# Optimization experiments

Hardware: AMD Instinct MI355X
Metric: run time of the kernel (lower is better)

## Reference

```python
import jax, jax.numpy as jnp
import numpy as np

D = 1024
H = 16
HD = D // H
E = 64
K = 2


def setup_inputs() -> dict:
    key = jax.random.key(0)
    ks = jax.random.split(key, 10)
    s = 0.02
    return {
        "x": jax.random.normal(ks[0], (8, 2048, D), dtype=jnp.float32),
        "expert_embeddings": jax.random.normal(ks[1], (E, D), dtype=jnp.float32),
        "in_proj_w": jax.random.normal(ks[2], (3 * D, D), dtype=jnp.float32) * s,
        "in_proj_b": jax.random.normal(ks[3], (3 * D,), dtype=jnp.float32) * s,
        "out_proj_w": jax.random.normal(ks[4], (D, D), dtype=jnp.float32) * s,
        "out_proj_b": jax.random.normal(ks[5], (D,), dtype=jnp.float32) * s,
        "gate_w1": jax.random.normal(ks[6], (4 * E, D), dtype=jnp.float32) * s,
        "gate_b1": jax.random.normal(ks[7], (4 * E,), dtype=jnp.float32) * s,
        "gate_w2": jax.random.normal(ks[8], (E, 4 * E), dtype=jnp.float32) * s,
        "gate_b2": jax.random.normal(ks[9], (E,), dtype=jnp.float32) * s,
    }


def reference(x, expert_embeddings, in_proj_w, in_proj_b, out_proj_w, out_proj_b,
              gate_w1, gate_b1, gate_w2, gate_b2):
    B, S, _ = x.shape
    wq, wk, wv = jnp.split(in_proj_w, 3, axis=0)   # each (D, D)
    bq, bk, bv = jnp.split(in_proj_b, 3, axis=0)
    # cross-attention: queries from x, keys/values from expert embeddings (shared across batch)
    q = (x @ wq.T + bq).reshape(B, S, H, HD)                      # (B,S,H,hd)
    k = (expert_embeddings @ wk.T + bk).reshape(E, H, HD)         # (E,H,hd)
    v = (expert_embeddings @ wv.T + bv).reshape(E, H, HD)
    scores = jnp.einsum('bshd,ehd->bhse', q, k) / jnp.sqrt(jnp.float32(HD))
    attn = jax.nn.softmax(scores, axis=-1)                        # (B,H,S,E)
    o = jnp.einsum('bhse,ehd->bshd', attn, v).reshape(B, S, D)
    attn_out = o @ out_proj_w.T + out_proj_b                      # (B,S,D)
    # gate MLP (exact GELU like torch default)
    h = jax.nn.gelu(attn_out @ gate_w1.T + gate_b1, approximate=False)
    gate_logits = h @ gate_w2.T + gate_b2                         # (B,S,E)
    probs = jax.nn.softmax(gate_logits, axis=-1)
    vals, idx = jax.lax.top_k(probs, K)                           # (B,S,K)
    weights = vals / (jnp.sum(vals, axis=-1, keepdims=True) + 1e-8)
    return idx, weights
```

## Files before the change

### kernel.cpp

```cpp
#include <hip/hip_runtime.h>
#include <math.h>


typedef _Float16 h8 __attribute__((ext_vector_type(8)));
typedef _Float16 h4 __attribute__((ext_vector_type(4)));
typedef float f4 __attribute__((ext_vector_type(4)));

__device__ __forceinline__ float gelu_exact(float x) {
    return 0.5f * x * (1.0f + erff(x * 0.70710678118654752f));
}

__global__ __launch_bounds__(256) void split2_kernel(
    const float* __restrict__ src, _Float16* __restrict__ dst, long total, int colsh) {
    long i = ((long)blockIdx.x * 256 + threadIdx.x) * 4;
    if (i >= total) return;
    f4 v = *(const f4*)(src + i);
    long row = i >> colsh; int col = (int)(i & ((1 << colsh) - 1));
    _Float16* d0 = dst + (row << (colsh + 1)) + col;
    h4 lo, hi;
    #pragma unroll
    for (int j = 0; j < 4; j++) {
        _Float16 a = (_Float16)v[j];
        lo[j] = a;
        hi[j] = (_Float16)((v[j] - (float)a) * 4096.0f);
    }
    *(h4*)d0 = lo;
    *(h4*)(d0 + (1 << colsh)) = hi;
}

__global__ __launch_bounds__(256) void kv_kernel(
    const float* __restrict__ w, const float* __restrict__ b,
    const float* __restrict__ ee, float* __restrict__ kbuf, float* __restrict__ vtbuf) {
    __shared__ float As[32][68];
    __shared__ float Bs[32][68];
    int tid = threadIdx.x;
    int r0 = blockIdx.x * 64;
    int tx = tid & 15, ty = tid >> 4;
    float acc[4][4] = {};
    const float* wbase = w + (size_t)(1024 + r0) * 1024;
    for (int k0 = 0; k0 < 1024; k0 += 32) {
        #pragma unroll
        for (int i = 0; i < 2; i++) {
            int f = tid + i * 256;
            int row = f >> 3, c4 = f & 7;
            float4 v = *(const float4*)(wbase + (size_t)row * 1024 + k0 + c4 * 4);
            As[c4*4+0][row] = v.x; As[c4*4+1][row] = v.y;
            As[c4*4+2][row] = v.z; As[c4*4+3][row] = v.w;
            float4 u = *(const float4*)(ee + (size_t)row * 1024 + k0 + c4 * 4);
            Bs[c4*4+0][row] = u.x; Bs[c4*4+1][row] = u.y;
            Bs[c4*4+2][row] = u.z; Bs[c4*4+3][row] = u.w;
        }
        __syncthreads();
        #pragma unroll
        for (int kk = 0; kk < 32; kk++) {
            float a[4], bb[4];
            *(float4*)&a[0]  = *(const float4*)&As[kk][ty * 4];
            *(float4*)&bb[0] = *(const float4*)&Bs[kk][tx * 4];
            #pragma unroll
            for (int i = 0; i < 4; i++)
                #pragma unroll
                for (int j = 0; j < 4; j++)
                    acc[i][j] = fmaf(a[i], bb[j], acc[i][j]);
        }
        __syncthreads();
    }
    #pragma unroll
    for (int i = 0; i < 4; i++) {
        int row = r0 + ty * 4 + i;
        float bias = b[1024 + row];
        int j = row & 1023;
        int h = j >> 6, hd = j & 63;
        #pragma unroll
        for (int jj = 0; jj < 4; jj++) {
            int e = tx * 4 + jj;
            float val = acc[i][jj] + bias;
            if (row < 1024) kbuf[h * 4096 + e * 64 + hd] = val;
            else            vtbuf[h * 4096 + hd * 64 + e] = val;
        }
    }
}

template<int GELU, int OSPLIT, int AF32>
__global__ __launch_bounds__(256, 2) void hgemm_kernel(
    const void* __restrict__ Av, const _Float16* __restrict__ B,
    const float* __restrict__ bias, void* __restrict__ Cv, int ldc, int nhalf) {
    __shared__ __align__(16) _Float16 As[128 * 32];
    __shared__ __align__(16) _Float16 Ah[128 * 32];
    __shared__ __align__(16) _Float16 Bl[128 * 32];
    __shared__ __align__(16) _Float16 Bh[128 * 32];
    int tid = threadIdx.x;

    int gx = gridDim.x;
    int nwg = gx * gridDim.y;
    int lid = blockIdx.y * gx + blockIdx.x;
    int L = (lid & 7) * (nwg >> 3) + (lid >> 3);
    int m0 = (L / gx) * 128, n0 = (L % gx) * 128;

    int w = tid >> 6, l = tid & 63;
    int wm = w & 1, wn = w >> 1;
    int lr = l & 15, lk = l >> 4;

    f4 acc1[4][4], acc2[4][4];
    #pragma unroll
    for (int i = 0; i < 4; i++)
        #pragma unroll
        for (int j = 0; j < 4; j++) {
            acc1[i][j] = (f4){0.f, 0.f, 0.f, 0.f};
            acc2[i][j] = (f4){0.f, 0.f, 0.f, 0.f};
        }

    int r0 = tid >> 2, c0 = tid & 3;
    int s0 = r0 * 32 + c0 * 8, s1 = s0 + 64 * 32;
    int rb = tid >> 3, c4 = tid & 7;

    const _Float16* Ab = (const _Float16*)Av + (size_t)m0 * 2048;
    const float*    Af = (const float*)Av + (size_t)m0 * 1024;
    const _Float16* Bb = B + (size_t)n0 * 2048;

    float4 xa[4];
    uint4 ua0, ua1, uh0, uh1, ub0, ub1, uc0, uc1;
    if (AF32) {
        #pragma unroll
        for (int f = 0; f < 4; f++)
            xa[f] = *(const float4*)(Af + (size_t)(rb + f * 32) * 1024 + c4 * 4);
    } else {
        ua0 = *(const uint4*)(Ab + (size_t)r0 * 2048 + c0 * 8);
        ua1 = *(const uint4*)(Ab + (size_t)(r0 + 64) * 2048 + c0 * 8);
        uh0 = *(const uint4*)(Ab + (size_t)r0 * 2048 + 1024 + c0 * 8);
        uh1 = *(const uint4*)(Ab + (size_t)(r0 + 64) * 2048 + 1024 + c0 * 8);
    }
    ub0 = *(const uint4*)(Bb + (size_t)r0 * 2048 + c0 * 8);
    ub1 = *(const uint4*)(Bb + (size_t)(r0 + 64) * 2048 + c0 * 8);
    uc0 = *(const uint4*)(Bb + (size_t)r0 * 2048 + 1024 + c0 * 8);
    uc1 = *(const uint4*)(Bb + (size_t)(r0 + 64) * 2048 + 1024 + c0 * 8);

    for (int kt = 0; kt < 32; kt++) {
        __syncthreads();
        if (AF32) {
            #pragma unroll
            for (int f = 0; f < 4; f++) {
                h4 lo, hi;
                #pragma unroll
                for (int j = 0; j < 4; j++) {
                    float v = ((const float*)&xa[f])[j];
                    _Float16 a = (_Float16)v;
                    lo[j] = a;
                    hi[j] = (_Float16)((v - (float)a) * 4096.0f);
                }
                *(h4*)(As + (rb + f * 32) * 32 + c4 * 4) = lo;
                *(h4*)(Ah + (rb + f * 32) * 32 + c4 * 4) = hi;
            }
        } else {
            *(uint4*)(As + s0) = ua0; *(uint4*)(As + s1) = ua1;
            *(uint4*)(Ah + s0) = uh0; *(uint4*)(Ah + s1) = uh1;
        }
        *(uint4*)(Bl + s0) = ub0; *(uint4*)(Bl + s1) = ub1;
        *(uint4*)(Bh + s0) = uc0; *(uint4*)(Bh + s1) = uc1;
        __syncthreads();
        if (kt < 31) {
            int ka = (kt + 1) * 32;
            if (AF32) {
                #pragma unroll
                for (int f = 0; f < 4; f++)
                    xa[f] = *(const float4*)(Af + (size_t)(rb + f * 32) * 1024 + ka + c4 * 4);
            } else {
                ua0 = *(const uint4*)(Ab + (size_t)r0 * 2048 + ka + c0 * 8);
                ua1 = *(const uint4*)(Ab + (size_t)(r0 + 64) * 2048 + ka + c0 * 8);
                uh0 = *(const uint4*)(Ab + (size_t)r0 * 2048 + 1024 + ka + c0 * 8);
                uh1 = *(const uint4*)(Ab + (size_t)(r0 + 64) * 2048 + 1024 + ka + c0 * 8);
            }
            ub0 = *(const uint4*)(Bb + (size_t)r0 * 2048 + ka + c0 * 8);
            ub1 = *(const uint4*)(Bb + (size_t)(r0 + 64) * 2048 + ka + c0 * 8);
            uc0 = *(const uint4*)(Bb + (size_t)r0 * 2048 + 1024 + ka + c0 * 8);
            uc1 = *(const uint4*)(Bb + (size_t)(r0 + 64) * 2048 + 1024 + ka + c0 * 8);
        }
        h8 a1f[4], blf[4], bhf[4];
        #pragma unroll
        for (int mi = 0; mi < 4; mi++)
            a1f[mi] = *(const h8*)(As + (wm * 64 + mi * 16 + lr) * 32 + lk * 8);
        #pragma unroll
        for (int ni = 0; ni < 4; ni++) {
            blf[ni] = *(const h8*)(Bl + (wn * 64 + ni * 16 + lr) * 32 + lk * 8);
            bhf[ni] = *(const h8*)(Bh + (wn * 64 + ni * 16 + lr) * 32 + lk * 8);
        }
        #pragma unroll
        for (int mi = 0; mi < 4; mi++)
            #pragma unroll
            for (int ni = 0; ni < 4; ni++) {
                acc1[mi][ni] = __builtin_amdgcn_mfma_f32_16x16x32_f16(a1f[mi], blf[ni], acc1[mi][ni], 0, 0, 0);
                acc2[mi][ni] = __builtin_amdgcn_mfma_f32_16x16x32_f16(a1f[mi], bhf[ni], acc2[mi][ni], 0, 0, 0);
            }
        h8 a2f[4];
        #pragma unroll
        for (int mi = 0; mi < 4; mi++)
            a2f[mi] = *(const h8*)(Ah + (wm * 64 + mi * 16 + lr) * 32 + lk * 8);
        #pragma unroll
        for (int mi = 0; mi < 4; mi++)
            #pragma unroll
            for (int ni = 0; ni < 4; ni++)
                acc2[mi][ni] = __builtin_amdgcn_mfma_f32_16x16x32_f16(a2f[mi], blf[ni], acc2[mi][ni], 0, 0, 0);
    }

    #pragma unroll
    for (int mi = 0; mi < 4; mi++)
        #pragma unroll
        for (int ni = 0; ni < 4; ni++) {
            int n = n0 + wn * 64 + ni * 16 + lr;
            float bn = bias[n];
            #pragma unroll
            for (int j = 0; j < 4; j++) {
                int m = m0 + wm * 64 + mi * 16 + lk * 4 + j;
                float val = acc1[mi][ni][j] + acc2[mi][ni][j] * (1.0f / 4096.0f) + bn;
                if (GELU) val = gelu_exact(val);
                if (OSPLIT) {
                    _Float16* Ch = (_Float16*)Cv;
                    _Float16 lo = (_Float16)val;
                    Ch[(size_t)m * ldc + n] = lo;
                    Ch[(size_t)m * ldc + nhalf + n] = (_Float16)((val - (float)lo) * 4096.0f);
                } else {
                    ((float*)Cv)[(size_t)m * ldc + n] = val;
                }
            }
        }
}

__global__ __launch_bounds__(256) void attn2_kernel(
    const float* __restrict__ kbuf, const float* __restrict__ vtbuf,
    const float* __restrict__ q, _Float16* __restrict__ os) {
    __shared__ __align__(16) float qs[4][64][68];
    __shared__ __align__(16) float ps[4][2][64];
    int tid = threadIdx.x;
    int w = tid >> 6, l = tid & 63;
    int wid = blockIdx.x * 4 + w;
    int b = wid >> 9, h = (wid >> 5) & 15, t0 = (wid & 31) * 64;

    f4 kr[16], vt[16];
    const f4* kp = (const f4*)(kbuf + h * 4096 + l * 64);
    const f4* vp = (const f4*)(vtbuf + h * 4096 + l * 64);
    #pragma unroll
    for (int i = 0; i < 16; i++) { kr[i] = kp[i]; vt[i] = vp[i]; }

    const float* qbase = q + ((size_t)(b * 2048 + t0)) * 1024 + h * 64;
    #pragma unroll
    for (int it = 0; it < 16; it++) {
        int f = it * 64 + l;
        int r = f >> 4, c = f & 15;
        f4 v = *(const f4*)(qbase + (size_t)r * 1024 + c * 4);
        *(f4*)&qs[w][r][c * 4] = v;
    }

    for (int t = 0; t < 64; t++) {
        float s = 0.f;
        #pragma unroll
        for (int i = 0; i < 16; i++) {
            f4 qv = *(const f4*)&qs[w][t][i * 4];
            s = fmaf(qv[0], kr[i][0], s);
            s = fmaf(qv[1], kr[i][1], s);
            s = fmaf(qv[2], kr[i][2], s);
            s = fmaf(qv[3], kr[i][3], s);
        }
        s *= 0.125f;
        float ex = __expf(s);
        float sum = ex;
        #pragma unroll
        for (int off = 32; off; off >>= 1) sum += __shfl_xor(sum, off, 64);
        float p = ex / sum;
        ps[w][t & 1][l] = p;
        float o = 0.f;
        #pragma unroll
        for (int i = 0; i < 16; i++) {
            f4 pv = *(const f4*)&ps[w][t & 1][i * 4];
            o = fmaf(pv[0], vt[i][0], o);
            o = fmaf(pv[1], vt[i][1], o);
            o = fmaf(pv[2], vt[i][2], o);
            o = fmaf(pv[3], vt[i][3], o);
        }
        _Float16 o1 = (_Float16)o;
        _Float16 o2 = (_Float16)((o - (float)o1) * 4096.0f);
        size_t tok = (size_t)(b * 2048 + t0 + t);
        os[tok * 2048 + h * 64 + l] = o1;
        os[tok * 2048 + 1024 + h * 64 + l] = o2;
    }
}

__global__ __launch_bounds__(256) void gate2_kernel(
    const _Float16* __restrict__ h1s, const _Float16* __restrict__ w2s,
    const float* __restrict__ b2, float* __restrict__ out) {
    int tid = threadIdx.x;
    int w = tid >> 6, l = tid & 63;
    int lr = l & 15, lk = l >> 4;
    int trow = blockIdx.x * 64 + w * 16;

    f4 acc1[4], acc2[4], acc3[4];
    #pragma unroll
    for (int ni = 0; ni < 4; ni++) {
        acc1[ni] = (f4){0.f,0.f,0.f,0.f};
        acc2[ni] = (f4){0.f,0.f,0.f,0.f};
        acc3[ni] = (f4){0.f,0.f,0.f,0.f};
    }
    const _Float16* Arow = h1s + (size_t)(trow + lr) * 512;
    #pragma unroll
    for (int kt = 0; kt < 8; kt++) {
        h8 a1 = *(const h8*)(Arow + kt * 32 + lk * 8);
        h8 a2 = *(const h8*)(Arow + 256 + kt * 32 + lk * 8);
        #pragma unroll
        for (int ni = 0; ni < 4; ni++) {
            const _Float16* Brow = w2s + (size_t)(ni * 16 + lr) * 512;
            h8 b1 = *(const h8*)(Brow + kt * 32 + lk * 8);
            h8 bh = *(const h8*)(Brow + 256 + kt * 32 + lk * 8);
            acc1[ni] = __builtin_amdgcn_mfma_f32_16x16x32_f16(a1, b1, acc1[ni], 0, 0, 0);
            acc2[ni] = __builtin_amdgcn_mfma_f32_16x16x32_f16(a1, bh, acc2[ni], 0, 0, 0);
            acc2[ni] = __builtin_amdgcn_mfma_f32_16x16x32_f16(a2, b1, acc2[ni], 0, 0, 0);
            acc3[ni] = __builtin_amdgcn_mfma_f32_16x16x32_f16(a2, bh, acc3[ni], 0, 0, 0);
        }
    }
    float bcol[4];
    #pragma unroll
    for (int ni = 0; ni < 4; ni++) bcol[ni] = b2[ni * 16 + lr];

    const float c1 = 1.0f / 4096.0f, c2 = 1.0f / 16777216.0f;
    #pragma unroll
    for (int j = 0; j < 4; j++) {
        int tok = trow + lk * 4 + j;
        float lg[4];
        #pragma unroll
        for (int ni = 0; ni < 4; ni++)
            lg[ni] = acc1[ni][j] + acc2[ni][j] * c1 + acc3[ni][j] * c2 + bcol[ni];
        float mx = fmaxf(fmaxf(lg[0], lg[1]), fmaxf(lg[2], lg[3]));
        #pragma unroll
        for (int off = 1; off <= 8; off <<= 1) mx = fmaxf(mx, __shfl_xor(mx, off, 64));
        float pr[4], s = 0.f;
        #pragma unroll
        for (int ni = 0; ni < 4; ni++) { pr[ni] = expf(lg[ni] - mx); s += pr[ni]; }
        #pragma unroll
        for (int off = 1; off <= 8; off <<= 1) s += __shfl_xor(s, off, 64);
        float inv = 1.0f / s;
        float v1 = -1.f, v2 = -1.f; int i1 = 0, i2 = 0;
        #pragma unroll
        for (int ni = 0; ni < 4; ni++) {
            float p = pr[ni] * inv;
            int e = ni * 16 + lr;
            if (p > v1) { v2 = v1; i2 = i1; v1 = p; i1 = e; }
            else if (p > v2) { v2 = p; i2 = e; }
        }
        #pragma unroll
        for (int off = 1; off <= 8; off <<= 1) {
            float u1 = __shfl_xor(v1, off, 64); int k1 = __shfl_xor(i1, off, 64);
            float u2 = __shfl_xor(v2, off, 64); int k2 = __shfl_xor(i2, off, 64);
            if (u1 > v1) {
                if (v1 > u2) { v2 = v1; i2 = i1; } else { v2 = u2; i2 = k2; }
                v1 = u1; i1 = k1;
            } else if (u1 > v2) { v2 = u1; i2 = k1; }
        }
        if (lr == 0) {
            float wsum = v1 + v2 + 1e-8f;
            out[(size_t)tok * 2]     = (float)i1;
            out[(size_t)tok * 2 + 1] = (float)i2;
            out[32768 + (size_t)tok * 2]     = v1 / wsum;
            out[32768 + (size_t)tok * 2 + 1] = v2 / wsum;
        }
    }
}

extern "C" void kernel_launch(void* const* d_in, const int* in_sizes, int n_in,
                              void* d_out, int out_size, void* d_ws, size_t ws_size,
                              hipStream_t stream) {
    const float* x   = (const float*)d_in[0];
    const float* ee  = (const float*)d_in[1];
    const float* ipw = (const float*)d_in[2];
    const float* ipb = (const float*)d_in[3];
    const float* opw = (const float*)d_in[4];
    const float* opb = (const float*)d_in[5];
    const float* gw1 = (const float*)d_in[6];
    const float* gb1 = (const float*)d_in[7];
    const float* gw2 = (const float*)d_in[8];
    const float* gb2 = (const float*)d_in[9];
    float* out = (float*)d_out;
    char* ws = (char*)d_ws;

    _Float16* os    = (_Float16*)ws;
    _Float16* h1s   = (_Float16*)ws;
    float*    qbuf  = (float*)(ws + 67108864);
    _Float16* aos   = (_Float16*)(ws + 67108864);
    _Float16* wqs   = (_Float16*)(ws + 134217728);
    _Float16* opws  = (_Float16*)(ws + 138412032);
    _Float16* gw1s  = (_Float16*)(ws + 142606336);
    float*    kbuf  = (float*)(ws + 143654912);
    _Float16* gw2s  = (_Float16*)(ws + 143654912);
    float*    vtbuf = (float*)(ws + 143917056);

    split2_kernel<<<dim3(1024), dim3(256), 0, stream>>>(ipw, wqs, 1048576L, 10);
    split2_kernel<<<dim3(1024), dim3(256), 0, stream>>>(opw, opws, 1048576L, 10);
    split2_kernel<<<dim3(256),  dim3(256), 0, stream>>>(gw1, gw1s, 262144L, 10);
    kv_kernel<<<dim3(32), dim3(256), 0, stream>>>(ipw, ipb, ee, kbuf, vtbuf);
    hgemm_kernel<0,0,1><<<dim3(8, 128), dim3(256), 0, stream>>>(x, wqs, ipb, qbuf, 1024, 0);
    attn2_kernel<<<dim3(1024), dim3(256), 0, stream>>>(kbuf, vtbuf, qbuf, os);
    split2_kernel<<<dim3(16), dim3(256), 0, stream>>>(gw2, gw2s, 16384L, 8);
    hgemm_kernel<0,1,0><<<dim3(8, 128), dim3(256), 0, stream>>>(os, opws, opb, (void*)aos, 2048, 1024);
    hgemm_kernel<1,1,0><<<dim3(2, 128), dim3(256), 0, stream>>>(aos, gw1s, gb1, (void*)h1s, 512, 256);
    gate2_kernel<<<dim3(256), dim3(256), 0, stream>>>(h1s, gw2s, gb2, out);
}
```

Measured before the change: 570.5 us.

## Double-buffer LDS tiles in split-fp16 GEMM with one barrier per k-step

```diff
diff --git a/kernel.cpp b/kernel.cpp
--- a/kernel.cpp
+++ b/kernel.cpp
@@ -5,6 +5,11 @@
 typedef _Float16 h8 __attribute__((ext_vector_type(8)));
 typedef _Float16 h4 __attribute__((ext_vector_type(4)));
 typedef float f4 __attribute__((ext_vector_type(4)));
+
+#define BAR() do { \
+    asm volatile("s_waitcnt lgkmcnt(0)" ::: "memory"); \
+    __builtin_amdgcn_s_barrier(); \
+    __builtin_amdgcn_sched_barrier(0); } while (0)
 
 __device__ __forceinline__ float gelu_exact(float x) {
     return 0.5f * x * (1.0f + erff(x * 0.70710678118654752f));
@@ -84,10 +89,8 @@
 __global__ __launch_bounds__(256, 2) void hgemm_kernel(
     const void* __restrict__ Av, const _Float16* __restrict__ B,
     const float* __restrict__ bias, void* __restrict__ Cv, int ldc, int nhalf) {
-    __shared__ __align__(16) _Float16 As[128 * 32];
-    __shared__ __align__(16) _Float16 Ah[128 * 32];
-    __shared__ __align__(16) _Float16 Bl[128 * 32];
-    __shared__ __align__(16) _Float16 Bh[128 * 32];
+    __shared__ __align__(16) _Float16 lds[2][4][128 * 32];
+    const int NT = 32;
     int tid = threadIdx.x;
 
     int gx = gridDim.x;
@@ -119,87 +122,85 @@
 
     float4 xa[4];
     uint4 ua0, ua1, uh0, uh1, ub0, ub1, uc0, uc1;
-    if (AF32) {
-        #pragma unroll
-        for (int f = 0; f < 4; f++)
-            xa[f] = *(const float4*)(Af + (size_t)(rb + f * 32) * 1024 + c4 * 4);
-    } else {
-        ua0 = *(const uint4*)(Ab + (size_t)r0 * 2048 + c0 * 8);
-        ua1 = *(const uint4*)(Ab + (size_t)(r0 + 64) * 2048 + c0 * 8);
-        uh0 = *(const uint4*)(Ab + (size_t)r0 * 2048 + 1024 + c0 * 8);
-        uh1 = *(const uint4*)(Ab + (size_t)(r0 + 64) * 2048 + 1024 + c0 * 8);
-    }
-    ub0 = *(const uint4*)(Bb + (size_t)r0 * 2048 + c0 * 8);
-    ub1 = *(const uint4*)(Bb + (size_t)(r0 + 64) * 2048 + c0 * 8);
-    uc0 = *(const uint4*)(Bb + (size_t)r0 * 2048 + 1024 + c0 * 8);
-    uc1 = *(const uint4*)(Bb + (size_t)(r0 + 64) * 2048 + 1024 + c0 * 8);
-
-    for (int kt = 0; kt < 32; kt++) {
-        __syncthreads();
-        if (AF32) {
-            #pragma unroll
-            for (int f = 0; f < 4; f++) {
-                h4 lo, hi;
-                #pragma unroll
-                for (int j = 0; j < 4; j++) {
-                    float v = ((const float*)&xa[f])[j];
-                    _Float16 a = (_Float16)v;
-                    lo[j] = a;
-                    hi[j] = (_Float16)((v - (float)a) * 4096.0f);
-                }
-                *(h4*)(As + (rb + f * 32) * 32 + c4 * 4) = lo;
-                *(h4*)(Ah + (rb + f * 32) * 32 + c4 * 4) = hi;
-            }
-        } else {
-            *(uint4*)(As + s0) = ua0; *(uint4*)(As + s1) = ua1;
-            *(uint4*)(Ah + s0) = uh0; *(uint4*)(Ah + s1) = uh1;
-        }
-        *(uint4*)(Bl + s0) = ub0; *(uint4*)(Bl + s1) = ub1;
-        *(uint4*)(Bh + s0) = uc0; *(uint4*)(Bh + s1) = uc1;
-        __syncthreads();
-        if (kt < 31) {
-            int ka = (kt + 1) * 32;
-            if (AF32) {
-                #pragma unroll
-                for (int f = 0; f < 4; f++)
-                    xa[f] = *(const float4*)(Af + (size_t)(rb + f * 32) * 1024 + ka + c4 * 4);
-            } else {
-                ua0 = *(const uint4*)(Ab + (size_t)r0 * 2048 + ka + c0 * 8);
-                ua1 = *(const uint4*)(Ab + (size_t)(r0 + 64) * 2048 + ka + c0 * 8);
-                uh0 = *(const uint4*)(Ab + (size_t)r0 * 2048 + 1024 + ka + c0 * 8);
-                uh1 = *(const uint4*)(Ab + (size_t)(r0 + 64) * 2048 + 1024 + ka + c0 * 8);
-            }
-            ub0 = *(const uint4*)(Bb + (size_t)r0 * 2048 + ka + c0 * 8);
-            ub1 = *(const uint4*)(Bb + (size_t)(r0 + 64) * 2048 + ka + c0 * 8);
-            uc0 = *(const uint4*)(Bb + (size_t)r0 * 2048 + 1024 + ka + c0 * 8);
-            uc1 = *(const uint4*)(Bb + (size_t)(r0 + 64) * 2048 + 1024 + ka + c0 * 8);
-        }
-        h8 a1f[4], blf[4], bhf[4];
-        #pragma unroll
-        for (int mi = 0; mi < 4; mi++)
-            a1f[mi] = *(const h8*)(As + (wm * 64 + mi * 16 + lr) * 32 + lk * 8);
+
+#define LOADT(kt) do { int ka_ = (kt) * 32;                                         \
+    if (AF32) {                                                                     \
+        _Pragma("unroll")                                                           \
+        for (int f = 0; f < 4; f++)                                                 \
+            xa[f] = *(const float4*)(Af + (size_t)(rb + f * 32) * 1024 + ka_ + c4 * 4); \
+    } else {                                                                        \
+        ua0 = *(const uint4*)(Ab + (size_t)r0 * 2048 + ka_ + c0 * 8);               \
+        ua1 = *(const uint4*)(Ab + (size_t)(r0 + 64) * 2048 + ka_ + c0 * 8);        \
+        uh0 = *(const uint4*)(Ab + (size_t)r0 * 2048 + 1024 + ka_ + c0 * 8);        \
+        uh1 = *(const uint4*)(Ab + (size_t)(r0 + 64) * 2048 + 1024 + ka_ + c0 * 8); \
+    }                                                                               \
+    ub0 = *(const uint4*)(Bb + (size_t)r0 * 2048 + ka_ + c0 * 8);                   \
+    ub1 = *(const uint4*)(Bb + (size_t)(r0 + 64) * 2048 + ka_ + c0 * 8);            \
+    uc0 = *(const uint4*)(Bb + (size_t)r0 * 2048 + 1024 + ka_ + c0 * 8);            \
+    uc1 = *(const uint4*)(Bb + (size_t)(r0 + 64) * 2048 + 1024 + ka_ + c0 * 8);     \
+} while (0)
+
+#define WRITET(bi) do {                                                             \
+    if (AF32) {                                                                     \
+        _Pragma("unroll")                                                           \
+        for (int f = 0; f < 4; f++) {                                               \
+            h4 lo_, hi_;                                                            \
+            _Pragma("unroll")                                                       \
+            for (int j = 0; j < 4; j++) {                                           \
+                float v_ = ((const float*)&xa[f])[j];                               \
+                _Float16 a_ = (_Float16)v_;                                         \
+                lo_[j] = a_;                                                        \
+                hi_[j] = (_Float16)((v_ - (float)a_) * 4096.0f);                    \
+            }                                                                       \
+            *(h4*)(&lds[bi][0][0] + (rb + f * 32) * 32 + c4 * 4) = lo_;             \
+            *(h4*)(&lds[bi][1][0] + (rb + f * 32) * 32 + c4 * 4) = hi_;             \
+        }                                                                           \
+    } else {                                                                        \
+        *(uint4*)(&lds[bi][0][0] + s0) = ua0; *(uint4*)(&lds[bi][0][0] + s1) = ua1; \
+        *(uint4*)(&lds[bi][1][0] + s0) = uh0; *(uint4*)(&lds[bi][1][0] + s1) = uh1; \
+    }                                                                               \
+    *(uint4*)(&lds[bi][2][0] + s0) = ub0; *(uint4*)(&lds[bi][2][0] + s1) = ub1;     \
+    *(uint4*)(&lds[bi][3][0] + s0) = uc0; *(uint4*)(&lds[bi][3][0] + s1) = uc1;     \
+} while (0)
+
+    LOADT(0);
+    WRITET(0);
+    LOADT(1);
+    BAR();
+
+    for (int t = 0; t < NT; t++) {
+        int cur = t & 1;
+        if (t + 1 < NT) WRITET(cur ^ 1);
+        if (t + 2 < NT) LOADT(t + 2);
+        const _Float16* L0 = &lds[cur][0][0];
+        const _Float16* L1 = &lds[cur][1][0];
+        const _Float16* L2 = &lds[cur][2][0];
+        const _Float16* L3 = &lds[cur][3][0];
+        h8 a1f[4], blf[4], bhf[4], a2f[4];
+        #pragma unroll
+        for (int mi = 0; mi < 4; mi++) {
+            a1f[mi] = *(const h8*)(L0 + (wm * 64 + mi * 16 + lr) * 32 + lk * 8);
+            a2f[mi] = *(const h8*)(L1 + (wm * 64 + mi * 16 + lr) * 32 + lk * 8);
+        }
         #pragma unroll
         for (int ni = 0; ni < 4; ni++) {
-            blf[ni] = *(const h8*)(Bl + (wn * 64 + ni * 16 + lr) * 32 + lk * 8);
-            bhf[ni] = *(const h8*)(Bh + (wn * 64 + ni * 16 + lr) * 32 + lk * 8);
-        }
+            blf[ni] = *(const h8*)(L2 + (wn * 64 + ni * 16 + lr) * 32 + lk * 8);
+            bhf[ni] = *(const h8*)(L3 + (wn * 64 + ni * 16 + lr) * 32 + lk * 8);
+        }
+        __builtin_amdgcn_s_setprio(1);
         #pragma unroll
         for (int mi = 0; mi < 4; mi++)
             #pragma unroll
             for (int ni = 0; ni < 4; ni++) {
                 acc1[mi][ni] = __builtin_amdgcn_mfma_f32_16x16x32_f16(a1f[mi], blf[ni], acc1[mi][ni], 0, 0, 0);
                 acc2[mi][ni] = __builtin_amdgcn_mfma_f32_16x16x32_f16(a1f[mi], bhf[ni], acc2[mi][ni], 0, 0, 0);
+                acc2[mi][ni] = __builtin_amdgcn_mfma_f32_16x16x32_f16(a2f[mi], blf[ni], acc2[mi][ni], 0, 0, 0);
             }
-        h8 a2f[4];
-        #pragma unroll
-        for (int mi = 0; mi < 4; mi++)
-            a2f[mi] = *(const h8*)(Ah + (wm * 64 + mi * 16 + lr) * 32 + lk * 8);
-        #pragma unroll
-        for (int mi = 0; mi < 4; mi++)
-            #pragma unroll
-            for (int ni = 0; ni < 4; ni++)
-                acc2[mi][ni] = __builtin_amdgcn_mfma_f32_16x16x32_f16(a2f[mi], blf[ni], acc2[mi][ni], 0, 0, 0);
-    }
+        __builtin_amdgcn_s_setprio(0);
+        BAR();
+    }
+#undef LOADT
+#undef WRITET
 
     #pragma unroll
     for (int mi = 0; mi < 4; mi++)
```

Result: faster. 550.8 us (-3.5%).
